# Performance work log

Measured on AMD Instinct MI355X. Metric: run time of the kernel, lower is better.

The kernel has to match this reference:

```python
import jax, jax.numpy as jnp
import numpy as np

D_MODEL = 2048
HEADS = 16


def setup_inputs() -> dict:
    key = jax.random.key(0)
    ks = jax.random.split(key, 9)
    s = 1.0 / np.sqrt(D_MODEL)
    x = jax.random.normal(ks[0], (2, 2048, D_MODEL), dtype=jnp.float32)
    wq = jax.random.uniform(ks[1], (D_MODEL, D_MODEL), jnp.float32, -s, s)
    wk = jax.random.uniform(ks[2], (D_MODEL, D_MODEL), jnp.float32, -s, s)
    wv = jax.random.uniform(ks[3], (D_MODEL, D_MODEL), jnp.float32, -s, s)
    wo = jax.random.uniform(ks[4], (D_MODEL, D_MODEL), jnp.float32, -s, s)
    bq = jax.random.uniform(ks[5], (D_MODEL,), jnp.float32, -s, s)
    bk = jax.random.uniform(ks[6], (D_MODEL,), jnp.float32, -s, s)
    bv = jax.random.uniform(ks[7], (D_MODEL,), jnp.float32, -s, s)
    bo = jax.random.uniform(ks[8], (D_MODEL,), jnp.float32, -s, s)
    return {"x": x, "wq": wq, "bq": bq, "wk": wk, "bk": bk,
            "wv": wv, "bv": bv, "wo": wo, "bo": bo}


def _split(t, heads):
    b, s, d = t.shape
    return t.reshape(b, s, heads, d // heads).transpose(0, 2, 1, 3)  # [b,h,s,dh]


def reference(x, wq, bq, wk, bk, wv, bv, wo, bo):
    q = x @ wq.T + bq
    k = x @ wk.T + bk
    v = x @ wv.T + bv
    q, k, v = _split(q, HEADS), _split(k, HEADS), _split(v, HEADS)
    dh = q.shape[-1]
    scale = 1.0 / np.sqrt(dh).astype(np.float32)
    score = jnp.einsum('bhqd,bhkd->bhqk', q, k) * scale  # [b,h,s,s]
    score = jax.nn.softmax(score.astype(jnp.float32), axis=-1).astype(q.dtype)
    out = jnp.einsum('bhqk,bhkd->bhqd', score, v)
    b, h, s, _ = out.shape
    out = out.transpose(0, 2, 1, 3).reshape(b, s, h * dh)
    return out @ wo.T + bo
```

## Files before the change

kernel.cpp:

```cpp
#include <hip/hip_runtime.h>
#include <cstdint>
#include <cstddef>

#define D_MODEL 2048
#define SEQ 2048
#define BATCH 2
#define HEADS 16
#define DH 128
#define MROWS (BATCH * SEQ)

typedef __attribute__((ext_vector_type(8))) short short8;
typedef __attribute__((ext_vector_type(4))) float f32x4;
typedef __attribute__((ext_vector_type(16))) float f32x16;
typedef __attribute__((ext_vector_type(2))) unsigned int uint2e;

__device__ __forceinline__ unsigned short f2bf(float f) {
    unsigned int u = __builtin_bit_cast(unsigned int, f);
    u += 0x7fffu + ((u >> 16) & 1u);
    return (unsigned short)(u >> 16);
}

__device__ __forceinline__ unsigned int cvt_pk_bf16(float lo, float hi) {
    unsigned int w;
    asm("v_cvt_pk_bf16_f32 %0, %1, %2" : "=v"(w) : "v"(lo), "v"(hi));
    return w;
}

__device__ __forceinline__ void swap32(unsigned int& x, unsigned int& y) {
#if __has_builtin(__builtin_amdgcn_permlane32_swap)
    uint2e r = __builtin_amdgcn_permlane32_swap(x, y, false, false);
    x = r[0]; y = r[1];
#else
    const int hi = (threadIdx.x >> 5) & 1;
    const unsigned int gx = (unsigned int)__shfl_xor((int)x, 32);
    const unsigned int gy = (unsigned int)__shfl_xor((int)y, 32);
    const unsigned int nx = hi ? gy : x;
    const unsigned int ny = hi ? y : gx;
    x = nx; y = ny;
#endif
}

__device__ __forceinline__ void gload_lds16(const unsigned short* g, unsigned short* l) {
    __builtin_amdgcn_global_load_lds(
        (const __attribute__((address_space(1))) void*)g,
        (__attribute__((address_space(3))) void*)l, 16, 0, 0);
}

__global__ __launch_bounds__(256) void cvt_kernel(const float* __restrict__ in,
                                                  unsigned short* __restrict__ out, int n4) {
    int i = blockIdx.x * 256 + threadIdx.x;
    if (i < n4) {
        const float4 v = reinterpret_cast<const float4*>(in)[i];
        ushort4 o;
        o.x = f2bf(v.x); o.y = f2bf(v.y); o.z = f2bf(v.z); o.w = f2bf(v.w);
        reinterpret_cast<ushort4*>(out)[i] = o;
    }
}

template <int MODE, typename OUT_T>
__global__ __launch_bounds__(256, 2)
void gemm_bt(const unsigned short* __restrict__ A, const unsigned short* __restrict__ B,
             const float* __restrict__ bias, OUT_T* __restrict__ C,
             int M, int N, int K) {
    constexpr int BM = 128, BN = 128, BK = 64;
    __shared__ unsigned short As[BM * BK];
    __shared__ unsigned short Bs[BN * BK];

    const int tid  = threadIdx.x;
    const int lane = tid & 63;
    const int wid  = tid >> 6;
    const int ntile = N / BN;
    const int mt = blockIdx.x / ntile;
    const int nt = blockIdx.x % ntile;
    const int m0 = mt * BM, n0 = nt * BN;

    f32x4 acc[4][4] = {};

    const int srow = wid * 32 + (lane >> 3);
    const int schk = lane & 7;
    const int wr = wid >> 1, wc = wid & 1;
    const int fr = lane & 15;
    const int fg = lane >> 4;

    for (int k0 = 0; k0 < K; k0 += BK) {
#pragma unroll
        for (int j = 0; j < 4; ++j) {
            const int row = srow + j * 8;
            const int gch = schk ^ (row & 7);
            gload_lds16(A + (size_t)(m0 + row) * K + k0 + gch * 8,
                        As + (wid * 32 + j * 8) * BK);
            gload_lds16(B + (size_t)(n0 + row) * K + k0 + gch * 8,
                        Bs + (wid * 32 + j * 8) * BK);
        }
        __syncthreads();
#pragma unroll
        for (int kk = 0; kk < 2; ++kk) {
            short8 af[4], bf[4];
#pragma unroll
            for (int i = 0; i < 4; ++i) {
                const int ra = wr * 64 + i * 16 + fr;
                af[i] = *(const short8*)&As[ra * BK + (((kk * 4) + fg) ^ (ra & 7)) * 8];
                const int rb = wc * 64 + i * 16 + fr;
                bf[i] = *(const short8*)&Bs[rb * BK + (((kk * 4) + fg) ^ (rb & 7)) * 8];
            }
#pragma unroll
            for (int mi = 0; mi < 4; ++mi)
#pragma unroll
                for (int ni = 0; ni < 4; ++ni)
                    acc[mi][ni] = __builtin_amdgcn_mfma_f32_16x16x32_bf16(
                        af[mi], bf[ni], acc[mi][ni], 0, 0, 0);
        }
        __syncthreads();
    }

#pragma unroll
    for (int mi = 0; mi < 4; ++mi) {
#pragma unroll
        for (int ni = 0; ni < 4; ++ni) {
            const int col = n0 + wc * 64 + ni * 16 + fr;
            const float bv = bias[col];
            if constexpr (MODE == 2) {
                const int row_b = m0 + wr * 64 + mi * 16 + fg * 4;
                ushort4 o4;
                o4.x = f2bf(acc[mi][ni][0] + bv);
                o4.y = f2bf(acc[mi][ni][1] + bv);
                o4.z = f2bf(acc[mi][ni][2] + bv);
                o4.w = f2bf(acc[mi][ni][3] + bv);
                *(ushort4*)&C[(size_t)col * M + row_b] = o4;
            } else {
#pragma unroll
                for (int r = 0; r < 4; ++r) {
                    const int row = m0 + wr * 64 + mi * 16 + fg * 4 + r;
                    const float v = acc[mi][ni][r] + bv;
                    if constexpr (MODE == 1) {
                        C[(size_t)row * N + col] = (OUT_T)f2bf(v);
                    } else {
                        C[(size_t)row * N + col] = v;
                    }
                }
            }
        }
    }
}

__global__ __launch_bounds__(256, 2)
void flash_attn3(const unsigned short* __restrict__ Q, const unsigned short* __restrict__ Kg,
                 const unsigned short* __restrict__ VT, unsigned short* __restrict__ O) {
    constexpr int KVB = 64;
    constexpr int NT = SEQ / KVB;
    __shared__ unsigned short Ks[2 * KVB * DH];
    __shared__ unsigned short Vs[2 * DH * KVB];

    const int tid  = threadIdx.x;
    const int lane = tid & 63;
    const int wid  = tid >> 6;
    const int l31  = lane & 31;
    const int hi   = lane >> 5;

    const int qt = blockIdx.x & 15;
    const int bh = blockIdx.x >> 4;
    const int b = bh >> 4, h = bh & 15;
    const int qrow = qt * 128 + wid * 32 + l31;

    const unsigned short* Qp = Q + ((size_t)b * SEQ + qrow) * D_MODEL + h * DH;
    const unsigned short* Kp = Kg + (size_t)b * SEQ * D_MODEL + h * DH;
    const unsigned short* Vp = VT + (size_t)(h * DH) * MROWS + (size_t)b * SEQ;

    short8 qf[8];
#pragma unroll
    for (int kk = 0; kk < 8; ++kk)
        qf[kk] = *(const short8*)(Qp + kk * 16 + hi * 8);

    f32x16 acc[4] = {};
    float m_run = -1e30f, l_run = 0.f;
    const float Cc = 0.088388347648318447f * 1.4426950408889634f;
    const float THR = 8.0f / Cc;

    int co[8];
#pragma unroll
    for (int kk = 0; kk < 8; ++kk) co[kk] = ((kk * 2 + hi) ^ (l31 & 7)) * 8;

    int kroff[4], vroff[4];
#pragma unroll
    for (int q = 0; q < 4; ++q) {
        const int row_l = wid * 16 + q * 4 + (lane >> 4);
        kroff[q] = row_l * D_MODEL + ((lane & 15) ^ (row_l & 7)) * 8;
        const int d_l = wid * 32 + q * 8 + (lane >> 3);
        vroff[q] = d_l * MROWS + ((lane & 7) ^ (d_l & 7)) * 8;
    }
    unsigned short* KsW = Ks + (wid * 16) * DH;
    unsigned short* VsW = Vs + (wid * 32) * KVB;

#pragma unroll
    for (int q = 0; q < 4; ++q) {
        gload_lds16(Kp + kroff[q], KsW + q * 4 * DH);
        gload_lds16(Vp + vroff[q], VsW + q * 8 * KVB);
    }
    __syncthreads();

    for (int t = 0; t < NT; ++t) {
        const int cur = t & 1;
        if (t + 1 < NT) {
            const unsigned short* Kt = Kp + (size_t)((t + 1) * KVB) * D_MODEL;
            const unsigned short* Vt = Vp + (t + 1) * KVB;
            unsigned short* kd = KsW + (cur ^ 1) * (KVB * DH);
            unsigned short* vd = VsW + (cur ^ 1) * (DH * KVB);
#pragma unroll
            for (int q = 0; q < 4; ++q) {
                gload_lds16(Kt + kroff[q], kd + q * 4 * DH);
                gload_lds16(Vt + vroff[q], vd + q * 8 * KVB);
            }
        }
        const unsigned short* Kc = Ks + cur * (KVB * DH);
        const unsigned short* Vc = Vs + cur * (DH * KVB);

        f32x16 st0 = {}, st1 = {};
        __builtin_amdgcn_s_setprio(1);
#pragma unroll
        for (int kk = 0; kk < 8; ++kk) {
            const short8 kf0 = *(const short8*)&Kc[l31 * DH + co[kk]];
            const short8 kf1 = *(const short8*)&Kc[(32 + l31) * DH + co[kk]];
            st0 = __builtin_amdgcn_mfma_f32_32x32x16_bf16(kf0, qf[kk], st0, 0, 0, 0);
            st1 = __builtin_amdgcn_mfma_f32_32x32x16_bf16(kf1, qf[kk], st1, 0, 0, 0);
        }
        __builtin_amdgcn_s_setprio(0);

        float lm = -1e30f;
#pragma unroll
        for (int r = 0; r < 16; ++r) lm = fmaxf(lm, fmaxf(st0[r], st1[r]));
        {
            unsigned int a = __builtin_bit_cast(unsigned int, lm), bb = a;
            swap32(a, bb);
            lm = fmaxf(lm, __builtin_bit_cast(float, hi ? a : bb));
        }
        if (__any(lm > m_run + THR)) {
            const float mn = fmaxf(m_run, lm);
            const float sf = __builtin_amdgcn_exp2f((m_run - mn) * Cc);
            m_run = mn;
            l_run *= sf;
#pragma unroll
            for (int db = 0; db < 4; ++db)
#pragma unroll
                for (int r = 0; r < 16; ++r) acc[db][r] *= sf;
        }
        const float mc = m_run * Cc;
        float p0[16], p1[16];
        float ps = 0.f;
#pragma unroll
        for (int r = 0; r < 16; ++r) {
            p0[r] = __builtin_amdgcn_exp2f(__builtin_fmaf(st0[r], Cc, -mc));
            p1[r] = __builtin_amdgcn_exp2f(__builtin_fmaf(st1[r], Cc, -mc));
            ps += p0[r] + p1[r];
        }
        {
            unsigned int a = __builtin_bit_cast(unsigned int, ps), bb = a;
            swap32(a, bb);
            ps += __builtin_bit_cast(float, hi ? a : bb);
        }
        l_run += ps;

        unsigned int W0[8], W1[8];
#pragma unroll
        for (int tt = 0; tt < 8; ++tt) {
            W0[tt] = cvt_pk_bf16(p0[2 * tt], p0[2 * tt + 1]);
            W1[tt] = cvt_pk_bf16(p1[2 * tt], p1[2 * tt + 1]);
        }
        swap32(W0[0], W0[2]); swap32(W0[1], W0[3]);
        swap32(W0[4], W0[6]); swap32(W0[5], W0[7]);
        swap32(W1[0], W1[2]); swap32(W1[1], W1[3]);
        swap32(W1[4], W1[6]); swap32(W1[5], W1[7]);
        short8 pf[4];
        {
            uint4 f;
            f.x = W0[0]; f.y = W0[1]; f.z = W0[2]; f.w = W0[3];
            pf[0] = __builtin_bit_cast(short8, f);
            f.x = W0[4]; f.y = W0[5]; f.z = W0[6]; f.w = W0[7];
            pf[1] = __builtin_bit_cast(short8, f);
            f.x = W1[0]; f.y = W1[1]; f.z = W1[2]; f.w = W1[3];
            pf[2] = __builtin_bit_cast(short8, f);
            f.x = W1[4]; f.y = W1[5]; f.z = W1[6]; f.w = W1[7];
            pf[3] = __builtin_bit_cast(short8, f);
        }

        __builtin_amdgcn_s_setprio(1);
#pragma unroll
        for (int db = 0; db < 4; ++db) {
#pragma unroll
            for (int kk16 = 0; kk16 < 4; ++kk16) {
                const short8 vf = *(const short8*)&Vc[(db * 32 + l31) * KVB + co[kk16]];
                acc[db] = __builtin_amdgcn_mfma_f32_32x32x16_bf16(vf, pf[kk16], acc[db], 0, 0, 0);
            }
        }
        __builtin_amdgcn_s_setprio(0);
        __syncthreads();
    }

    const float inv_l = 1.0f / l_run;
    unsigned short* Op = O + ((size_t)b * SEQ + qrow) * D_MODEL + h * DH;
#pragma unroll
    for (int db = 0; db < 4; ++db)
#pragma unroll
        for (int g = 0; g < 4; ++g) {
            ushort4 o4;
            o4.x = f2bf(acc[db][4 * g + 0] * inv_l);
            o4.y = f2bf(acc[db][4 * g + 1] * inv_l);
            o4.z = f2bf(acc[db][4 * g + 2] * inv_l);
            o4.w = f2bf(acc[db][4 * g + 3] * inv_l);
            *(ushort4*)(Op + db * 32 + g * 8 + hi * 4) = o4;
        }
}

extern "C" void kernel_launch(void* const* d_in, const int* in_sizes, int n_in,
                              void* d_out, int out_size, void* d_ws, size_t ws_size,
                              hipStream_t stream) {
    (void)in_sizes; (void)n_in; (void)out_size; (void)ws_size;
    const float* x  = (const float*)d_in[0];
    const float* wq = (const float*)d_in[1];
    const float* bq = (const float*)d_in[2];
    const float* wk = (const float*)d_in[3];
    const float* bk = (const float*)d_in[4];
    const float* wv = (const float*)d_in[5];
    const float* bv = (const float*)d_in[6];
    const float* wo = (const float*)d_in[7];
    const float* bo = (const float*)d_in[8];
    float* out = (float*)d_out;

    unsigned short* ws = (unsigned short*)d_ws;
    const size_t NX = (size_t)MROWS * D_MODEL;
    const size_t NW = (size_t)D_MODEL * D_MODEL;
    unsigned short* xb  = ws;
    unsigned short* wqb = xb + NX;
    unsigned short* wkb = wqb + NW;
    unsigned short* wvb = wkb + NW;
    unsigned short* wob = wvb + NW;
    unsigned short* Qb  = wob + NW;
    unsigned short* Kb  = Qb + NX;
    unsigned short* VTb = Kb + NX;
    unsigned short* Ab  = VTb + NX;

    cvt_kernel<<<(unsigned)(NX / 1024), 256, 0, stream>>>(x,  xb,  (int)(NX / 4));
    cvt_kernel<<<(unsigned)(NW / 1024), 256, 0, stream>>>(wq, wqb, (int)(NW / 4));
    cvt_kernel<<<(unsigned)(NW / 1024), 256, 0, stream>>>(wk, wkb, (int)(NW / 4));
    cvt_kernel<<<(unsigned)(NW / 1024), 256, 0, stream>>>(wv, wvb, (int)(NW / 4));
    cvt_kernel<<<(unsigned)(NW / 1024), 256, 0, stream>>>(wo, wob, (int)(NW / 4));

    gemm_bt<1, unsigned short><<<512, 256, 0, stream>>>(xb, wqb, bq, Qb, MROWS, D_MODEL, D_MODEL);
    gemm_bt<1, unsigned short><<<512, 256, 0, stream>>>(xb, wkb, bk, Kb, MROWS, D_MODEL, D_MODEL);
    gemm_bt<2, unsigned short><<<512, 256, 0, stream>>>(xb, wvb, bv, VTb, MROWS, D_MODEL, D_MODEL);

    flash_attn3<<<512, 256, 0, stream>>>(Qb, Kb, VTb, Ab);

    gemm_bt<0, float><<<512, 256, 0, stream>>>(Ab, wob, bo, out, MROWS, D_MODEL, D_MODEL);
}
```

Baseline: 280.4 us.

## Fuse QKV GEMMs into one double-buffered 512-thread GEMM and batch weight conversions

Replaces the three separate QKV projection GEMMs with a single launch covering the concatenated 6144-wide N dimension. The new GEMM uses 256x128 tiles with BK=32, 8 waves, double-buffered LDS with explicit vmcnt waits, s_setprio around the MFMAs, and an XCD-aware block remap. The four weight conversions are also merged into one kernel launch. The aim is to cut launch overhead and tail effects and to overlap global loads with MFMA work. In exchange it raises register and LDS pressure and relies on hand-placed waitcnt synchronisation being correct.

```diff
diff --git a/kernel.cpp b/kernel.cpp
--- a/kernel.cpp
+++ b/kernel.cpp
@@ -57,89 +57,172 @@
     }
 }
 
-template <int MODE, typename OUT_T>
-__global__ __launch_bounds__(256, 2)
-void gemm_bt(const unsigned short* __restrict__ A, const unsigned short* __restrict__ B,
-             const float* __restrict__ bias, OUT_T* __restrict__ C,
-             int M, int N, int K) {
-    constexpr int BM = 128, BN = 128, BK = 64;
-    __shared__ unsigned short As[BM * BK];
-    __shared__ unsigned short Bs[BN * BK];
+__global__ __launch_bounds__(256) void cvt4_kernel(const float* __restrict__ w0,
+                                                   const float* __restrict__ w1,
+                                                   const float* __restrict__ w2,
+                                                   const float* __restrict__ w3,
+                                                   unsigned short* __restrict__ out) {
+    const int per = (D_MODEL * D_MODEL) / 4;
+    int i = blockIdx.x * 256 + threadIdx.x;
+    const int sel = i / per;
+    const int off = i - sel * per;
+    const float* s = sel == 0 ? w0 : sel == 1 ? w1 : sel == 2 ? w2 : w3;
+    const float4 v = reinterpret_cast<const float4*>(s)[off];
+    ushort4 o;
+    o.x = f2bf(v.x); o.y = f2bf(v.y); o.z = f2bf(v.z); o.w = f2bf(v.w);
+    reinterpret_cast<ushort4*>(out)[i] = o;
+}
+
+template <int MODE>
+__global__ __launch_bounds__(512, 4)
+void gemm8(const unsigned short* __restrict__ A,
+           const unsigned short* __restrict__ W0,
+           const unsigned short* __restrict__ W1,
+           const unsigned short* __restrict__ W2,
+           const float* __restrict__ b0f,
+           const float* __restrict__ b1f,
+           const float* __restrict__ b2f,
+           unsigned short* __restrict__ O0,
+           unsigned short* __restrict__ O1,
+           unsigned short* __restrict__ O2,
+           float* __restrict__ OF) {
+    constexpr int BM = 256, BN = 128, BK = 32;
+    constexpr int K = D_MODEL;
+    constexpr int NTILES = K / BK;
+    constexpr int NT_N = (MODE == 0 ? (3 * D_MODEL) / BN : D_MODEL / BN);
+    __shared__ unsigned short As[2][BM * BK];
+    __shared__ unsigned short Bs[2][BN * BK];
 
     const int tid  = threadIdx.x;
     const int lane = tid & 63;
     const int wid  = tid >> 6;
-    const int ntile = N / BN;
-    const int mt = blockIdx.x / ntile;
-    const int nt = blockIdx.x % ntile;
-    const int m0 = mt * BM, n0 = nt * BN;
+
+    constexpr int NWG = (MROWS / BM) * NT_N;
+    const int wk = (blockIdx.x & 7) * (NWG >> 3) + (blockIdx.x >> 3);
+    const int nt = wk % NT_N;
+    const int mt = wk / NT_N;
+    const int m0 = mt * BM;
+    const int n0 = nt * BN;
+
+    const unsigned short* Bw;
+    const float* bias;
+    int nloc;
+    if constexpr (MODE == 0) {
+        const int nsel = n0 >> 11;
+        nloc = n0 & 2047;
+        Bw = nsel == 0 ? W0 : (nsel == 1 ? W1 : W2);
+        bias = nsel == 0 ? b0f : (nsel == 1 ? b1f : b2f);
+    } else {
+        Bw = W0; bias = b0f; nloc = n0;
+    }
+
+    const int srow = lane >> 2;
+    const int schk = lane & 3;
+    const int r0 = wid * 16 + srow;
+    const int r1 = 128 + r0;
+    const unsigned short* aSrc0 = A  + (size_t)(m0 + r0) * K + (schk ^ (r0 & 3)) * 8;
+    const unsigned short* aSrc1 = A  + (size_t)(m0 + r1) * K + (schk ^ (r1 & 3)) * 8;
+    const unsigned short* bSrc  = Bw + (size_t)(nloc + r0) * K + (schk ^ (r0 & 3)) * 8;
+
+    const int fr = lane & 15, fg = lane >> 4;
+    const int wm = wid >> 1, wn = wid & 1;
+    const int ar = wm * 64 + fr;
+    const int br = wn * 64 + fr;
+    const int aoff = ar * BK + (fg ^ (ar & 3)) * 8;
+    const int boff = br * BK + (fg ^ (br & 3)) * 8;
 
     f32x4 acc[4][4] = {};
 
-    const int srow = wid * 32 + (lane >> 3);
-    const int schk = lane & 7;
-    const int wr = wid >> 1, wc = wid & 1;
-    const int fr = lane & 15;
-    const int fg = lane >> 4;
-
-    for (int k0 = 0; k0 < K; k0 += BK) {
-#pragma unroll
-        for (int j = 0; j < 4; ++j) {
-            const int row = srow + j * 8;
-            const int gch = schk ^ (row & 7);
-            gload_lds16(A + (size_t)(m0 + row) * K + k0 + gch * 8,
-                        As + (wid * 32 + j * 8) * BK);
-            gload_lds16(B + (size_t)(n0 + row) * K + k0 + gch * 8,
-                        Bs + (wid * 32 + j * 8) * BK);
-        }
-        __syncthreads();
-#pragma unroll
-        for (int kk = 0; kk < 2; ++kk) {
-            short8 af[4], bf[4];
-#pragma unroll
-            for (int i = 0; i < 4; ++i) {
-                const int ra = wr * 64 + i * 16 + fr;
-                af[i] = *(const short8*)&As[ra * BK + (((kk * 4) + fg) ^ (ra & 7)) * 8];
-                const int rb = wc * 64 + i * 16 + fr;
-                bf[i] = *(const short8*)&Bs[rb * BK + (((kk * 4) + fg) ^ (rb & 7)) * 8];
-            }
+#define STAGE(BUF, KOFF)                                                       \
+    gload_lds16(aSrc0 + (KOFF), &As[BUF][(wid * 16) * BK]);                    \
+    gload_lds16(aSrc1 + (KOFF), &As[BUF][(128 + wid * 16) * BK]);              \
+    gload_lds16(bSrc + (KOFF), &Bs[BUF][(wid * 16) * BK]);
+
+#define GBODY(T, BUF)                                                          \
+    {                                                                          \
+        if ((T) + 1 < NTILES) {                                                \
+            asm volatile("s_waitcnt vmcnt(3)" ::: "memory");                   \
+        } else {                                                               \
+            asm volatile("s_waitcnt vmcnt(0)" ::: "memory");                   \
+        }                                                                      \
+        __builtin_amdgcn_s_barrier();                                          \
+        asm volatile("" ::: "memory");                                         \
+        short8 af[4], bf[4];                                                   \
+        _Pragma("unroll")                                                      \
+        for (int mi = 0; mi < 4; ++mi)                                         \
+            af[mi] = *(const short8*)&As[BUF][aoff + mi * (16 * BK)];          \
+        _Pragma("unroll")                                                      \
+        for (int ni = 0; ni < 4; ++ni)                                         \
+            bf[ni] = *(const short8*)&Bs[BUF][boff + ni * (16 * BK)];          \
+        __builtin_amdgcn_s_setprio(1);                                         \
+        _Pragma("unroll")                                                      \
+        for (int mi = 0; mi < 4; ++mi)                                         \
+            _Pragma("unroll")                                                  \
+            for (int ni = 0; ni < 4; ++ni)                                     \
+                acc[mi][ni] = __builtin_amdgcn_mfma_f32_16x16x32_bf16(         \
+                    af[mi], bf[ni], acc[mi][ni], 0, 0, 0);                     \
+        __builtin_amdgcn_s_setprio(0);                                         \
+        asm volatile("s_waitcnt lgkmcnt(0)" ::: "memory");                     \
+        __builtin_amdgcn_s_barrier();                                          \
+        asm volatile("" ::: "memory");                                         \
+        if ((T) + 2 < NTILES) { STAGE(BUF, ((T) + 2) * BK) }                   \
+    }
+
+    STAGE(0, 0)
+    STAGE(1, BK)
+
+    for (int t = 0; t < NTILES; t += 2) {
+        GBODY(t, 0)
+        GBODY(t + 1, 1)
+    }
+#undef GBODY
+#undef STAGE
+
+    if constexpr (MODE == 0) {
+        const int nsel = n0 >> 11;
+        if (nsel == 2) {
 #pragma unroll
             for (int mi = 0; mi < 4; ++mi)
 #pragma unroll
-                for (int ni = 0; ni < 4; ++ni)
-                    acc[mi][ni] = __builtin_amdgcn_mfma_f32_16x16x32_bf16(
-                        af[mi], bf[ni], acc[mi][ni], 0, 0, 0);
-        }
-        __syncthreads();
-    }
-
-#pragma unroll
-    for (int mi = 0; mi < 4; ++mi) {
-#pragma unroll
-        for (int ni = 0; ni < 4; ++ni) {
-            const int col = n0 + wc * 64 + ni * 16 + fr;
-            const float bv = bias[col];
-            if constexpr (MODE == 2) {
-                const int row_b = m0 + wr * 64 + mi * 16 + fg * 4;
-                ushort4 o4;
-                o4.x = f2bf(acc[mi][ni][0] + bv);
-                o4.y = f2bf(acc[mi][ni][1] + bv);
-                o4.z = f2bf(acc[mi][ni][2] + bv);
-                o4.w = f2bf(acc[mi][ni][3] + bv);
-                *(ushort4*)&C[(size_t)col * M + row_b] = o4;
-            } else {
-#pragma unroll
-                for (int r = 0; r < 4; ++r) {
-                    const int row = m0 + wr * 64 + mi * 16 + fg * 4 + r;
-                    const float v = acc[mi][ni][r] + bv;
-                    if constexpr (MODE == 1) {
-                        C[(size_t)row * N + col] = (OUT_T)f2bf(v);
-                    } else {
-                        C[(size_t)row * N + col] = v;
+                for (int ni = 0; ni < 4; ++ni) {
+                    const int col = nloc + wn * 64 + ni * 16 + fr;
+                    const int row0 = m0 + wm * 64 + mi * 16 + fg * 4;
+                    const float bv = bias[col];
+                    ushort4 o4;
+                    o4.x = f2bf(acc[mi][ni][0] + bv);
+                    o4.y = f2bf(acc[mi][ni][1] + bv);
+                    o4.z = f2bf(acc[mi][ni][2] + bv);
+                    o4.w = f2bf(acc[mi][ni][3] + bv);
+                    *(ushort4*)&O2[(size_t)col * MROWS + row0] = o4;
+                }
+        } else {
+            unsigned short* Co = nsel ? O1 : O0;
+#pragma unroll
+            for (int mi = 0; mi < 4; ++mi)
+#pragma unroll
+                for (int ni = 0; ni < 4; ++ni) {
+                    const int col = nloc + wn * 64 + ni * 16 + fr;
+                    const float bv = bias[col];
+#pragma unroll
+                    for (int r = 0; r < 4; ++r) {
+                        const int row = m0 + wm * 64 + mi * 16 + fg * 4 + r;
+                        Co[(size_t)row * D_MODEL + col] = f2bf(acc[mi][ni][r] + bv);
                     }
                 }
+        }
+    } else {
+#pragma unroll
+        for (int mi = 0; mi < 4; ++mi)
+#pragma unroll
+            for (int ni = 0; ni < 4; ++ni) {
+                const int col = nloc + wn * 64 + ni * 16 + fr;
+                const float bv = bias[col];
+#pragma unroll
+                for (int r = 0; r < 4; ++r) {
+                    const int row = m0 + wm * 64 + mi * 16 + fg * 4 + r;
+                    OF[(size_t)row * D_MODEL + col] = acc[mi][ni][r] + bv;
+                }
             }
-        }
     }
 }
 
@@ -338,17 +421,14 @@
     unsigned short* VTb = Kb + NX;
     unsigned short* Ab  = VTb + NX;
 
-    cvt_kernel<<<(unsigned)(NX / 1024), 256, 0, stream>>>(x,  xb,  (int)(NX / 4));
-    cvt_kernel<<<(unsigned)(NW / 1024), 256, 0, stream>>>(wq, wqb, (int)(NW / 4));
-    cvt_kernel<<<(unsigned)(NW / 1024), 256, 0, stream>>>(wk, wkb, (int)(NW / 4));
-    cvt_kernel<<<(unsigned)(NW / 1024), 256, 0, stream>>>(wv, wvb, (int)(NW / 4));
-    cvt_kernel<<<(unsigned)(NW / 1024), 256, 0, stream>>>(wo, wob, (int)(NW / 4));
-
-    gemm_bt<1, unsigned short><<<512, 256, 0, stream>>>(xb, wqb, bq, Qb, MROWS, D_MODEL, D_MODEL);
-    gemm_bt<1, unsigned short><<<512, 256, 0, stream>>>(xb, wkb, bk, Kb, MROWS, D_MODEL, D_MODEL);
-    gemm_bt<2, unsigned short><<<512, 256, 0, stream>>>(xb, wvb, bv, VTb, MROWS, D_MODEL, D_MODEL);
+    cvt_kernel<<<(unsigned)(NX / 1024), 256, 0, stream>>>(x, xb, (int)(NX / 4));
+    cvt4_kernel<<<(unsigned)(4 * NW / 1024), 256, 0, stream>>>(wq, wk, wv, wo, wqb);
+
+    gemm8<0><<<768, 512, 0, stream>>>(xb, wqb, wkb, wvb, bq, bk, bv,
+                                      Qb, Kb, VTb, nullptr);
 
     flash_attn3<<<512, 256, 0, stream>>>(Qb, Kb, VTb, Ab);
 
-    gemm_bt<0, float><<<512, 256, 0, stream>>>(Ab, wob, bo, out, MROWS, D_MODEL, D_MODEL);
-}
+    gemm8<1><<<256, 512, 0, stream>>>(Ab, wob, nullptr, nullptr, bo, nullptr, nullptr,
+                                      nullptr, nullptr, nullptr, out);
+}
```

Measured after the change: 297.7 us. 6.2% more time.
